# Performance work log

Measured on AMD Instinct MI355X. Metric: run time of the kernel, lower is better.

The kernel has to match this reference:

```python
import jax, jax.numpy as jnp
import numpy as np

BS, C_IN, S1 = 64, 256, 32
D_OUT, J = 32, 10          # out_dim, num_out_caps (as_final_output -> spatial_size_2)
I = S1 * S1                # num_in_caps = 1024
ROUTE_NUM = 3


def setup_inputs() -> dict:
    key = jax.random.key(0)
    k1, k2, k3 = jax.random.split(key, 3)
    x = jax.random.normal(k1, (BS, C_IN, S1, S1), dtype=jnp.float32)
    W = jax.random.normal(k2, (D_OUT * J, C_IN), dtype=jnp.float32) * 0.02  # 1x1 conv weight
    W_b = jax.random.normal(k3, (D_OUT * J,), dtype=jnp.float32) * 0.02     # conv bias
    return {"x": x, "W": W, "W_b": W_b}


def squash(vec):
    # vec: [bs, j, d]; coeff = ||v||^2 / (1+||v||^2) / ||v||
    norm = jnp.linalg.norm(vec, axis=2, keepdims=True)
    norm_sq = norm * norm
    return vec * (norm_sq / (1.0 + norm_sq) / norm)


def reference(x, W, W_b):
    bs = x.shape[0]
    # 1x1 conv == per-pixel matmul: [bs, J*D, h, w]
    pred = jnp.einsum('bchw,oc->bohw', x, W) + W_b[None, :, None, None]
    # torch: resize(bs, J, D, I) on contiguous tensor, then permute(0,3,1,2)
    pred = pred.reshape(bs, J, D_OUT, I).transpose(0, 3, 1, 2)  # [bs, I, J, D]
    b = jnp.zeros((bs, J, I), dtype=x.dtype)  # b_init='zero'
    v = None
    for _ in range(ROUTE_NUM):
        c = jax.nn.softmax(b, axis=1)                    # softmax over output caps j
        s = jnp.einsum('bji,bijd->bjd', c, pred)          # per-capsule weighted sum
        v = squash(s)                                     # [bs, J, D]
        delta_b = jnp.einsum('bjd,bijd->bji', v, pred)    # agreement
        b = b + jax.lax.stop_gradient(delta_b)            # torch .detach()
    return v  # as_final_output=True -> [bs, J, D]
```

## Files before the change

### kernel.cpp

```cpp
#include <hip/hip_runtime.h>
#include <hip/hip_bf16.h>

typedef __attribute__((ext_vector_type(8))) unsigned short u16x8;
typedef __attribute__((ext_vector_type(4))) unsigned short u16x4;
typedef __attribute__((ext_vector_type(8))) short short8;
typedef __attribute__((ext_vector_type(4))) float floatx4;

#define BS 64
#define CIN 256
#define II 1024
#define OO 320
#define JJ 10
#define DD 32

__device__ __forceinline__ float b2f(unsigned short u) {
    union { unsigned int i; float f; } x; x.i = ((unsigned int)u) << 16; return x.f;
}
__device__ __forceinline__ float b2f_lo(unsigned int v) {
    union { unsigned int i; float f; } x; x.i = v << 16; return x.f;
}
__device__ __forceinline__ float b2f_hi(unsigned int v) {
    union { unsigned int i; float f; } x; x.i = v & 0xffff0000u; return x.f;
}
__device__ __forceinline__ unsigned short f2b(float f) {
    union { float f; unsigned int i; } x; x.f = f;
    unsigned int r = x.i + 0x7fffu + ((x.i >> 16) & 1u);
    return (unsigned short)(r >> 16);
}
__device__ __forceinline__ float redlm(float v) {
    v += __shfl_xor(v, 1); v += __shfl_xor(v, 2);
    v += __shfl_xor(v, 4); v += __shfl_xor(v, 8);
    return v;
}
__device__ __forceinline__ float redwave(float v) {
    v += __shfl_xor(v, 1);  v += __shfl_xor(v, 2);  v += __shfl_xor(v, 4);
    v += __shfl_xor(v, 8);  v += __shfl_xor(v, 16); v += __shfl_xor(v, 32);
    return v;
}

__global__ __launch_bounds__(256) void k_prepW(const float* __restrict__ W,
                                               unsigned short* __restrict__ Wl) {
    int gid = blockIdx.x * 256 + threadIdx.x;
    int lm = gid & 15;
    int quad = (gid >> 4) & 3;
    int mtl = (gid >> 6) & 3;
    int ks = (gid >> 8) & 7;
    int oc = gid >> 11;
    const float* src = W + (size_t)(oc * 64 + mtl * 16 + lm) * CIN + ks * 32 + quad * 8;
    float4 v0 = *(const float4*)src;
    float4 v1 = *(const float4*)(src + 4);
    u16x8 u;
    u[0] = f2b(v0.x); u[1] = f2b(v0.y); u[2] = f2b(v0.z); u[3] = f2b(v0.w);
    u[4] = f2b(v1.x); u[5] = f2b(v1.y); u[6] = f2b(v1.z); u[7] = f2b(v1.w);
    *(u16x8*)(Wl + (size_t)gid * 8) = u;
}

__global__ __launch_bounds__(512) void k_gemm6(const float* __restrict__ x,
                                               const unsigned short* __restrict__ Wl,
                                               const float* __restrict__ Wb,
                                               unsigned short* __restrict__ pred,
                                               float* __restrict__ psum0) {
    __shared__ unsigned short Bs[128 * 132];
    __shared__ unsigned short AsF[2048 * 8];
    __shared__ float ws_lds[8][OO];
    __shared__ float Wb_lds[OO];

    const int ic = blockIdx.x, b = blockIdx.y;
    const int t = threadIdx.x, w = t >> 6, l = t & 63;
    const int lm = l & 15, quad = l >> 4;
    const int i0 = ic * 128;

    if (t < OO) Wb_lds[t] = Wb[t];

    short8 bfrag[8];
    const int crow = t >> 5;
    const int f4 = t & 31;
#pragma unroll
    for (int kc = 0; kc < 2; ++kc) {
        float4 fr[8];
#pragma unroll
        for (int p = 0; p < 8; ++p) {
            int c = kc * 128 + p * 16 + crow;
            fr[p] = *(const float4*)(x + ((size_t)b * CIN + c) * II + i0 + 4 * f4);
        }
#pragma unroll
        for (int p = 0; p < 8; ++p) {
            int cl = p * 16 + crow;
            u16x4 u;
            u[0] = f2b(fr[p].x); u[1] = f2b(fr[p].y); u[2] = f2b(fr[p].z); u[3] = f2b(fr[p].w);
            *(u16x4*)&Bs[cl * 132 + 4 * f4] = u;
        }
        __syncthreads();
#pragma unroll
        for (int k2 = 0; k2 < 4; ++k2) {
            short8 f;
#pragma unroll
            for (int j = 0; j < 8; ++j)
                f[j] = (short)Bs[(k2 * 32 + quad * 8 + j) * 132 + w * 16 + lm];
            bfrag[kc * 4 + k2] = f;
        }
        __syncthreads();
    }

    const int ibase = i0 + w * 16 + lm;
#pragma unroll 1
    for (int oc = 0; oc < 5; ++oc) {
        if (oc > 0) __syncthreads();
        {
            const u16x8* src = (const u16x8*)Wl + oc * 2048;
            u16x8* dst = (u16x8*)AsF;
            for (int u = t; u < 2048; u += 512) dst[u] = src[u];
        }
        __syncthreads();

        floatx4 acc[4] = {};
#pragma unroll
        for (int ks = 0; ks < 8; ++ks)
#pragma unroll
            for (int mtl = 0; mtl < 4; ++mtl) {
                short8 af = *(const short8*)(AsF + (size_t)(((ks * 4 + mtl) * 4 + quad) * 16 + lm) * 8);
                acc[mtl] = __builtin_amdgcn_mfma_f32_16x16x32_bf16(af, bfrag[ks], acc[mtl], 0, 0, 0);
            }

#pragma unroll
        for (int mtl = 0; mtl < 4; ++mtl)
#pragma unroll
            for (int r = 0; r < 4; ++r) {
                int o = oc * 64 + mtl * 16 + quad * 4 + r;
                float v = acc[mtl][r] + Wb_lds[o];
                pred[((size_t)b * OO + o) * II + ibase] = f2b(v);
                float rs = redlm(v);
                if (lm == 0) ws_lds[w][o] = rs;
            }
    }
    __syncthreads();
    for (int u = t; u < OO; u += 512) {
        float s = 0.f;
#pragma unroll
        for (int ww = 0; ww < 8; ++ww) s += ws_lds[ww][u];
        psum0[((size_t)ic * BS + b) * OO + u] = s;
    }
}

__global__ __launch_bounds__(640) void k_route1(const float* __restrict__ psum0,
                                                const unsigned short* __restrict__ pred,
                                                float* __restrict__ blogG,
                                                float* __restrict__ psum1) {
    __shared__ float s_lds[OO];
    __shared__ float v_lds[OO];
    __shared__ float cf[JJ];
    __shared__ float dbuf[JJ][128];

    const int ic = blockIdx.x, b = blockIdx.y;
    const int t = threadIdx.x, w = t >> 6, l = t & 63;

    unsigned int vals[DD];
    {
        const unsigned short* pb = pred + ((size_t)b * OO + w * DD) * II + ic * 128 + 2 * l;
#pragma unroll
        for (int d = 0; d < DD; ++d) vals[d] = *(const unsigned int*)(pb + (size_t)d * II);
    }

    if (t < OO) {
        float s = 0.f;
#pragma unroll
        for (int sl = 0; sl < 8; ++sl) s += psum0[((size_t)sl * BS + b) * OO + t];
        s_lds[t] = 0.1f * s;
    }
    __syncthreads();
    if (t < JJ) {
        float n2 = 0.f;
#pragma unroll
        for (int d = 0; d < DD; ++d) { float v = s_lds[t * DD + d]; n2 += v * v; }
        cf[t] = sqrtf(n2) / (1.0f + n2);
    }
    __syncthreads();
    if (t < OO) v_lds[t] = s_lds[t] * cf[t >> 5];
    __syncthreads();

    float d0 = 0.f, d1 = 0.f;
#pragma unroll
    for (int d = 0; d < DD; ++d) {
        float vv = v_lds[w * DD + d];
        d0 += vv * b2f_lo(vals[d]);
        d1 += vv * b2f_hi(vals[d]);
    }
    *(float2*)(blogG + ((size_t)b * JJ + w) * II + ic * 128 + 2 * l) = make_float2(d0, d1);
    dbuf[w][2 * l] = d0; dbuf[w][2 * l + 1] = d1;
    __syncthreads();

    if (t < 128) {
        float lg[JJ];
#pragma unroll
        for (int j = 0; j < JJ; ++j) lg[j] = dbuf[j][t];
        float m = lg[0];
#pragma unroll
        for (int j = 1; j < JJ; ++j) m = fmaxf(m, lg[j]);
        float Z = 0.f, c[JJ];
#pragma unroll
        for (int j = 0; j < JJ; ++j) { c[j] = __expf(lg[j] - m); Z += c[j]; }
        float inv = 1.0f / Z;
#pragma unroll
        for (int j = 0; j < JJ; ++j) dbuf[j][t] = c[j] * inv;
    }
    __syncthreads();

    float c0 = dbuf[w][2 * l], c1 = dbuf[w][2 * l + 1];
#pragma unroll
    for (int d = 0; d < DD; ++d) {
        float p = c0 * b2f_lo(vals[d]) + c1 * b2f_hi(vals[d]);
        p = redwave(p);
        if (l == 0) psum1[((size_t)ic * BS + b) * OO + w * DD + d] = p;
    }
}

__global__ __launch_bounds__(640) void k_route2(const float* __restrict__ psum1,
                                                const unsigned short* __restrict__ pred,
                                                const float* __restrict__ blogG,
                                                float* __restrict__ psum2) {
    __shared__ float s_lds[OO];
    __shared__ float v_lds[OO];
    __shared__ float cf[JJ];
    __shared__ float dbuf[JJ][128];

    const int ic = blockIdx.x, b = blockIdx.y;
    const int t = threadIdx.x, w = t >> 6, l = t & 63;

    unsigned int vals[DD];
    {
        const unsigned short* pb = pred + ((size_t)b * OO + w * DD) * II + ic * 128 + 2 * l;
#pragma unroll
        for (int d = 0; d < DD; ++d) vals[d] = *(const unsigned int*)(pb + (size_t)d * II);
    }

    if (t < OO) {
        float s = 0.f;
#pragma unroll
        for (int sl = 0; sl < 8; ++sl) s += psum1[((size_t)sl * BS + b) * OO + t];
        s_lds[t] = s;
    }
    __syncthreads();
    if (t < JJ) {
        float n2 = 0.f;
#pragma unroll
        for (int d = 0; d < DD; ++d) { float v = s_lds[t * DD + d]; n2 += v * v; }
        cf[t] = sqrtf(n2) / (1.0f + n2);
    }
    __syncthreads();
    if (t < OO) v_lds[t] = s_lds[t] * cf[t >> 5];
    __syncthreads();

    float d0 = 0.f, d1 = 0.f;
#pragma unroll
    for (int d = 0; d < DD; ++d) {
        float vv = v_lds[w * DD + d];
        d0 += vv * b2f_lo(vals[d]);
        d1 += vv * b2f_hi(vals[d]);
    }
    float2 bl = *(const float2*)(blogG + ((size_t)b * JJ + w) * II + ic * 128 + 2 * l);
    dbuf[w][2 * l] = bl.x + d0; dbuf[w][2 * l + 1] = bl.y + d1;
    __syncthreads();

    if (t < 128) {
        float lg[JJ];
#pragma unroll
        for (int j = 0; j < JJ; ++j) lg[j] = dbuf[j][t];
        float m = lg[0];
#pragma unroll
        for (int j = 1; j < JJ; ++j) m = fmaxf(m, lg[j]);
        float Z = 0.f, c[JJ];
#pragma unroll
        for (int j = 0; j < JJ; ++j) { c[j] = __expf(lg[j] - m); Z += c[j]; }
        float inv = 1.0f / Z;
#pragma unroll
        for (int j = 0; j < JJ; ++j) dbuf[j][t] = c[j] * inv;
    }
    __syncthreads();

    float c0 = dbuf[w][2 * l], c1 = dbuf[w][2 * l + 1];
#pragma unroll
    for (int d = 0; d < DD; ++d) {
        float p = c0 * b2f_lo(vals[d]) + c1 * b2f_hi(vals[d]);
        p = redwave(p);
        if (l == 0) psum2[((size_t)ic * BS + b) * OO + w * DD + d] = p;
    }
}

__global__ __launch_bounds__(320) void k_final2(const float* __restrict__ psum2,
                                                float* __restrict__ out) {
    __shared__ float s_lds[OO];
    __shared__ float cf[JJ];
    int b = blockIdx.x, t = threadIdx.x;
    float s = 0.f;
#pragma unroll
    for (int sl = 0; sl < 8; ++sl) s += psum2[((size_t)sl * BS + b) * OO + t];
    s_lds[t] = s;
    __syncthreads();
    if (t < JJ) {
        float n2 = 0.f;
#pragma unroll
        for (int d = 0; d < DD; ++d) { float v = s_lds[t * DD + d]; n2 += v * v; }
        cf[t] = sqrtf(n2) / (1.0f + n2);
    }
    __syncthreads();
    out[b * OO + t] = s_lds[t] * cf[t >> 5];
}

extern "C" void kernel_launch(void* const* d_in, const int* in_sizes, int n_in,
                              void* d_out, int out_size, void* d_ws, size_t ws_size,
                              hipStream_t stream) {
    const float* x  = (const float*)d_in[0];
    const float* W  = (const float*)d_in[1];
    const float* Wb = (const float*)d_in[2];

    char* ws = (char*)d_ws;
    unsigned short* pred = (unsigned short*)ws;
    unsigned short* Wl   = (unsigned short*)(ws + 41943040);
    float* psum0 = (float*)(ws + 42106880);
    float* psum1 = (float*)(ws + 42762240);
    float* psum2 = (float*)(ws + 43417600);
    float* blogG = (float*)(ws + 44072960);

    k_prepW<<<40, 256, 0, stream>>>(W, Wl);
    k_gemm6<<<dim3(8, BS), 512, 0, stream>>>(x, Wl, Wb, pred, psum0);
    k_route1<<<dim3(8, BS), 640, 0, stream>>>(psum0, pred, blogG, psum1);
    k_route2<<<dim3(8, BS), 640, 0, stream>>>(psum1, pred, blogG, psum2);
    k_final2<<<BS, 320, 0, stream>>>(psum2, (float*)d_out);
}
```

Measured before the change: 173.5 us.

## Compute first routing sum via column-sum of x and small GEMV

With uniform first-iteration coupling, the first capsule sum is linear in the column sums of x. The GEMM kernel now sums each input channel over its pixel tile instead of reducing the 320 outputs with shuffles and LDS. A new small kernel folds these sums through the fp32 weights plus bias to get s1. This removes the per-output shuffle reduction and the LDS partial buffer from the GEMM epilogue, at the cost of an extra kernel launch and a slightly different rounding path (bf16 x sums with fp32 W).

```diff
diff --git a/kernel.cpp b/kernel.cpp
--- a/kernel.cpp
+++ b/kernel.cpp
@@ -26,11 +26,6 @@
     union { float f; unsigned int i; } x; x.f = f;
     unsigned int r = x.i + 0x7fffu + ((x.i >> 16) & 1u);
     return (unsigned short)(r >> 16);
-}
-__device__ __forceinline__ float redlm(float v) {
-    v += __shfl_xor(v, 1); v += __shfl_xor(v, 2);
-    v += __shfl_xor(v, 4); v += __shfl_xor(v, 8);
-    return v;
 }
 __device__ __forceinline__ float redwave(float v) {
     v += __shfl_xor(v, 1);  v += __shfl_xor(v, 2);  v += __shfl_xor(v, 4);
@@ -55,14 +50,13 @@
     *(u16x8*)(Wl + (size_t)gid * 8) = u;
 }
 
-__global__ __launch_bounds__(512) void k_gemm6(const float* __restrict__ x,
+__global__ __launch_bounds__(512) void k_gemm7(const float* __restrict__ x,
                                                const unsigned short* __restrict__ Wl,
                                                const float* __restrict__ Wb,
                                                unsigned short* __restrict__ pred,
-                                               float* __restrict__ psum0) {
+                                               float* __restrict__ psumC) {
     __shared__ unsigned short Bs[128 * 132];
     __shared__ unsigned short AsF[2048 * 8];
-    __shared__ float ws_lds[8][OO];
     __shared__ float Wb_lds[OO];
 
     const int ic = blockIdx.x, b = blockIdx.y;
@@ -73,8 +67,11 @@
     if (t < OO) Wb_lds[t] = Wb[t];
 
     short8 bfrag[8];
+    float csum[2];
     const int crow = t >> 5;
     const int f4 = t & 31;
+    const int cs_c = t >> 2;
+    const int cs_seg = t & 3;
 #pragma unroll
     for (int kc = 0; kc < 2; ++kc) {
         float4 fr[8];
@@ -99,7 +96,23 @@
                 f[j] = (short)Bs[(k2 * 32 + quad * 8 + j) * 132 + w * 16 + lm];
             bfrag[kc * 4 + k2] = f;
         }
+        {
+            float cs = 0.f;
+#pragma unroll
+            for (int q = 0; q < 8; ++q) {
+                u16x4 u = *(const u16x4*)&Bs[cs_c * 132 + cs_seg * 32 + q * 4];
+                cs += b2f(u[0]) + b2f(u[1]) + b2f(u[2]) + b2f(u[3]);
+            }
+            cs += __shfl_xor(cs, 1);
+            cs += __shfl_xor(cs, 2);
+            csum[kc] = cs;
+        }
         __syncthreads();
+    }
+    if (cs_seg == 0) {
+        size_t cbase = ((size_t)ic * BS + b) * CIN;
+        psumC[cbase + cs_c] = csum[0];
+        psumC[cbase + 128 + cs_c] = csum[1];
     }
 
     const int ibase = i0 + w * 16 + lm;
@@ -127,22 +140,35 @@
 #pragma unroll
             for (int r = 0; r < 4; ++r) {
                 int o = oc * 64 + mtl * 16 + quad * 4 + r;
-                float v = acc[mtl][r] + Wb_lds[o];
-                pred[((size_t)b * OO + o) * II + ibase] = f2b(v);
-                float rs = redlm(v);
-                if (lm == 0) ws_lds[w][o] = rs;
+                pred[((size_t)b * OO + o) * II + ibase] = f2b(acc[mtl][r] + Wb_lds[o]);
             }
     }
-    __syncthreads();
-    for (int u = t; u < OO; u += 512) {
+}
+
+__global__ __launch_bounds__(320) void k_gemv(const float* __restrict__ psumC,
+                                              const float* __restrict__ W,
+                                              const float* __restrict__ Wb,
+                                              float* __restrict__ s1) {
+    __shared__ float y_lds[CIN];
+    const int b = blockIdx.x, t = threadIdx.x;
+    if (t < CIN) {
         float s = 0.f;
 #pragma unroll
-        for (int ww = 0; ww < 8; ++ww) s += ws_lds[ww][u];
-        psum0[((size_t)ic * BS + b) * OO + u] = s;
-    }
-}
-
-__global__ __launch_bounds__(640) void k_route1(const float* __restrict__ psum0,
+        for (int sl = 0; sl < 8; ++sl) s += psumC[((size_t)sl * BS + b) * CIN + t];
+        y_lds[t] = s;
+    }
+    __syncthreads();
+    const float* wr = W + (size_t)t * CIN;
+    float acc = 0.f;
+#pragma unroll 4
+    for (int c = 0; c < CIN; c += 4) {
+        float4 wv = *(const float4*)(wr + c);
+        acc += wv.x * y_lds[c] + wv.y * y_lds[c + 1] + wv.z * y_lds[c + 2] + wv.w * y_lds[c + 3];
+    }
+    s1[(size_t)b * OO + t] = 0.1f * (acc + 1024.0f * Wb[t]);
+}
+
+__global__ __launch_bounds__(640) void k_route1(const float* __restrict__ s1,
                                                 const unsigned short* __restrict__ pred,
                                                 float* __restrict__ blogG,
                                                 float* __restrict__ psum1) {
@@ -161,12 +187,7 @@
         for (int d = 0; d < DD; ++d) vals[d] = *(const unsigned int*)(pb + (size_t)d * II);
     }
 
-    if (t < OO) {
-        float s = 0.f;
-#pragma unroll
-        for (int sl = 0; sl < 8; ++sl) s += psum0[((size_t)sl * BS + b) * OO + t];
-        s_lds[t] = 0.1f * s;
-    }
+    if (t < OO) s_lds[t] = s1[(size_t)b * OO + t];
     __syncthreads();
     if (t < JJ) {
         float n2 = 0.f;
@@ -316,14 +337,16 @@
     char* ws = (char*)d_ws;
     unsigned short* pred = (unsigned short*)ws;
     unsigned short* Wl   = (unsigned short*)(ws + 41943040);
-    float* psum0 = (float*)(ws + 42106880);
-    float* psum1 = (float*)(ws + 42762240);
-    float* psum2 = (float*)(ws + 43417600);
-    float* blogG = (float*)(ws + 44072960);
+    float* psumC = (float*)(ws + 42106880);
+    float* s1    = (float*)(ws + 42631168);
+    float* psum1 = (float*)(ws + 42713088);
+    float* psum2 = (float*)(ws + 43368448);
+    float* blogG = (float*)(ws + 44023808);
 
     k_prepW<<<40, 256, 0, stream>>>(W, Wl);
-    k_gemm6<<<dim3(8, BS), 512, 0, stream>>>(x, Wl, Wb, pred, psum0);
-    k_route1<<<dim3(8, BS), 640, 0, stream>>>(psum0, pred, blogG, psum1);
+    k_gemm7<<<dim3(8, BS), 512, 0, stream>>>(x, Wl, Wb, pred, psumC);
+    k_gemv<<<BS, 320, 0, stream>>>(psumC, W, Wb, s1);
+    k_route1<<<dim3(8, BS), 640, 0, stream>>>(s1, pred, blogG, psum1);
     k_route2<<<dim3(8, BS), 640, 0, stream>>>(psum1, pred, blogG, psum2);
     k_final2<<<BS, 320, 0, stream>>>(psum2, (float*)d_out);
 }
```

New measurement: 171.8 us. No clear change (-1.0%).
